# Performance work log

Measured on AMD Instinct MI355X. Metric: run time of the kernel, lower is better.

The kernel has to match this reference:

```python
import jax, jax.numpy as jnp
import numpy as np

B, S, D = 4, 2048, 1024
R = 64
N_FQK = N_FV = N_RQK = N_RV = 32
N_HEADS = 16
D_HEAD = D // N_HEADS


def setup_inputs() -> dict:
    key = jax.random.key(0)
    ks = jax.random.split(key, 10)

    def orth_bank(k, n, rows, cols):
        # mimic per-slice orthogonal init
        a = jax.random.normal(k, (n, rows, cols), dtype=jnp.float32)
        q, _ = jnp.linalg.qr(a) if rows >= cols else (jnp.swapaxes(jnp.linalg.qr(jnp.swapaxes(a, -1, -2))[0], -1, -2), None)
        return q.astype(jnp.float32)

    return {
        "x": jax.random.normal(ks[0], (B, S, D), dtype=jnp.float32),
        "fqk_weights": jax.random.uniform(ks[1], (B, S, N_FQK), dtype=jnp.float32),
        "fv_weights": jax.random.uniform(ks[2], (B, S, N_FV), dtype=jnp.float32),
        "rqk_weights_Q": jax.random.uniform(ks[3], (B, S, N_RQK), dtype=jnp.float32),
        "rqk_weights_K": jax.random.uniform(ks[4], (B, S, N_RQK), dtype=jnp.float32),
        "rv_weights": jax.random.uniform(ks[5], (B, S, N_RV), dtype=jnp.float32),
        "f_neurons": orth_bank(ks[6], N_FQK + N_FV, D, R),   # (64, D, R)
        "r_neurons": orth_bank(ks[7], N_RQK + N_RV, R, D),   # (64, R, D)
        "W_O": jax.random.normal(ks[8], (D, D), dtype=jnp.float32) * (1.0 / np.sqrt(D)),
    }


def reference(x, fqk_weights, fv_weights, rqk_weights_Q, rqk_weights_K, rv_weights,
              f_neurons, r_neurons, W_O):
    fqk = f_neurons[:N_FQK]          # (N, D, R)
    fv = f_neurons[N_FQK:]
    rqk = r_neurons[:N_RQK]          # (N, R, D)
    rv = r_neurons[N_RQK:]

    # Fused routed low-rank projections (same math as bsn,ndr->bsdr then bsd,bsdr->bsr,
    # reassociated to avoid the (B,S,D,R) intermediate).
    h_qk = jnp.einsum('bsd,bsn,ndr->bsr', x, fqk_weights, fqk)
    h_v = jnp.einsum('bsd,bsn,ndr->bsr', x, fv_weights, fv)

    Q = jnp.einsum('bsr,bsn,nrd->bsd', h_qk, rqk_weights_Q, rqk)
    K = jnp.einsum('bsr,bsn,nrd->bsd', h_qk, rqk_weights_K, rqk)
    V = jnp.einsum('bsr,bsn,nrd->bsd', h_v, rv_weights, rv)

    def heads(t):  # (B,S,D) -> (B,H,S,Dh)
        return t.reshape(B, S, N_HEADS, D_HEAD).transpose(0, 2, 1, 3)

    Qh, Kh, Vh = heads(Q), heads(K), heads(V)
    scores = jnp.einsum('bhqd,bhkd->bhqk', Qh, Kh) / np.sqrt(D_HEAD).astype(np.float32)
    causal = jnp.triu(jnp.ones((S, S), dtype=bool), k=1)
    scores = jnp.where(causal[None, None], -jnp.inf, scores)
    attn = jax.nn.softmax(scores, axis=-1)
    attn_out = jnp.einsum('bhqk,bhkd->bhqd', attn, Vh)
    attn_out = attn_out.transpose(0, 2, 1, 3).reshape(B, S, D)
    return attn_out @ W_O.T
```

## Files before the change

kernel.cpp:

```cpp
#include <hip/hip_runtime.h>
#include <hip/hip_bf16.h>


namespace {
constexpr int kS = 2048;
constexpr int kD = 1024;
}

typedef unsigned short u16;
typedef __attribute__((ext_vector_type(2))) float f32x2;
typedef __attribute__((ext_vector_type(4))) float f32x4;
typedef __attribute__((ext_vector_type(8))) short s8v;

union FragU { s8v s; unsigned u[4]; };
union F4U { f32x4 v; f32x2 p[2]; };

__device__ __forceinline__ u16 f2bf_bits(float f) {
  union { float f; unsigned u; } cv; cv.f = f;
  unsigned u = cv.u;
  unsigned r = u + 0x7fffu + ((u >> 16) & 1u);
  return (u16)(r >> 16);
}
__device__ __forceinline__ float bf2f(u16 b) {
  union { unsigned u; float f; } cv; cv.u = ((unsigned)b) << 16; return cv.f;
}
__device__ __forceinline__ unsigned pk_bf16(float a, float b) {
  __hip_bfloat162 h = __float22bfloat162_rn(make_float2(a, b));
  union { __hip_bfloat162 h; unsigned u; } cv; cv.h = h; return cv.u;
}
__device__ __forceinline__ void gl_lds16(const void* g, void* l) {
  __builtin_amdgcn_global_load_lds(
      (const __attribute__((address_space(1))) unsigned int*)g,
      (__attribute__((address_space(3))) unsigned int*)l, 16, 0, 0);
}

__global__ __launch_bounds__(256) void prep(
    const float* __restrict__ x, u16* __restrict__ xb,
    const float* __restrict__ f, u16* __restrict__ FT,
    const float* __restrict__ rn, u16* __restrict__ RT) {
  __shared__ float Tt[128 * 68];
  const int tid = threadIdx.x;
  const int bx = blockIdx.x;

  if (bx < 512) {
    float* T1 = Tt;
    const int d0 = (bx & 7) * 128;
    const int n  = bx >> 3;
#pragma unroll
    for (int e = 0; e < 8; ++e) {
      int flat = tid + e * 256;
      int dd = flat >> 4, r4 = (flat & 15) * 4;
      float4 v = *(const float4*)&f[((size_t)n * kD + d0 + dd) * 64 + r4];
      T1[(r4 + 0) * 132 + dd] = v.x;
      T1[(r4 + 1) * 132 + dd] = v.y;
      T1[(r4 + 2) * 132 + dd] = v.z;
      T1[(r4 + 3) * 132 + dd] = v.w;
    }
    __syncthreads();
#pragma unroll
    for (int e = 0; e < 4; ++e) {
      int flat = tid + e * 256;
      int r = flat >> 4, dq = (flat & 15) * 8;
      const float* p = &T1[r * 132 + dq];
      uint4 o = { pk_bf16(p[0], p[1]), pk_bf16(p[2], p[3]),
                  pk_bf16(p[4], p[5]), pk_bf16(p[6], p[7]) };
      *(uint4*)&FT[((size_t)n * 64 + r) * kD + d0 + dq] = o;
    }
  } else if (bx < 1024) {
    const int b2 = bx - 512;
    const int d0 = (b2 & 7) * 128;
    const int n  = b2 >> 3;
#pragma unroll
    for (int e = 0; e < 8; ++e) {
      int flat = tid + e * 256;
      int r = flat >> 5, d4 = (flat & 31) * 4;
      float4 v = *(const float4*)&rn[((size_t)n * 64 + r) * kD + d0 + d4];
      Tt[(d4 + 0) * 68 + r] = v.x;
      Tt[(d4 + 1) * 68 + r] = v.y;
      Tt[(d4 + 2) * 68 + r] = v.z;
      Tt[(d4 + 3) * 68 + r] = v.w;
    }
    __syncthreads();
#pragma unroll
    for (int e = 0; e < 4; ++e) {
      int flat = tid + e * 256;
      int dd = flat >> 3, rq = (flat & 7) * 8;
      const float* p = &Tt[dd * 68 + rq];
      uint4 o = { pk_bf16(p[0], p[1]), pk_bf16(p[2], p[3]),
                  pk_bf16(p[4], p[5]), pk_bf16(p[6], p[7]) };
      *(uint4*)&RT[((size_t)(d0 + dd)) * 4096 + n * 64 + rq] = o;
    }
  } else {
    int idx = (bx - 1024) * 256 + tid;
    float4 v0 = ((const float4*)x)[idx * 2];
    float4 v1 = ((const float4*)x)[idx * 2 + 1];
    uint4 o = { pk_bf16(v0.x, v0.y), pk_bf16(v0.z, v0.w),
                pk_bf16(v1.x, v1.y), pk_bf16(v1.z, v1.w) };
    ((uint4*)xb)[idx] = o;
  }
}

__global__ __launch_bounds__(256) void g_gemm(const u16* __restrict__ xb,
                                              const u16* __restrict__ FT,
                                              u16* __restrict__ G) {
  __shared__ short As[128 * 64];
  __shared__ short Bs[128 * 64];
  const int tid = threadIdx.x;
  const int lane = tid & 63, wid = tid >> 6;
  const int wm = wid & 1, wn = wid >> 1;
  const int quad = lane >> 4, l15 = lane & 15;
  const int cT = blockIdx.x * 128;
  const int tok0 = blockIdx.y * 128;

  f32x4 acc[4][4];
#pragma unroll
  for (int mt = 0; mt < 4; ++mt)
#pragma unroll
    for (int nt = 0; nt < 4; ++nt) acc[mt][nt] = {0.f, 0.f, 0.f, 0.f};

#pragma unroll 1
  for (int d0 = 0; d0 < kD; d0 += 64) {
    __syncthreads();
#pragma unroll
    for (int e = 0; e < 4; ++e) {
      int flat = tid + e * 256;
      int r = flat >> 3, u = (flat & 7) ^ (r & 7);
      gl_lds16(&xb[(size_t)(tok0 + r) * kD + d0 + u * 8], &As[flat * 8]);
    }
#pragma unroll
    for (int e = 0; e < 4; ++e) {
      int flat = tid + e * 256;
      int r = flat >> 3, u = (flat & 7) ^ (r & 7);
      gl_lds16(&FT[(size_t)(cT + r) * kD + d0 + u * 8], &Bs[flat * 8]);
    }
    __syncthreads();
    s8v a0[4], a1[4], b0[4], b1[4];
#pragma unroll
    for (int mt = 0; mt < 4; ++mt) {
      int r = wm * 64 + mt * 16 + l15;
      a0[mt] = *(const s8v*)&As[r * 64 + ((quad) ^ (r & 7)) * 8];
      a1[mt] = *(const s8v*)&As[r * 64 + ((4 + quad) ^ (r & 7)) * 8];
    }
#pragma unroll
    for (int nt = 0; nt < 4; ++nt) {
      int r = wn * 64 + nt * 16 + l15;
      b0[nt] = *(const s8v*)&Bs[r * 64 + ((quad) ^ (r & 7)) * 8];
      b1[nt] = *(const s8v*)&Bs[r * 64 + ((4 + quad) ^ (r & 7)) * 8];
    }
#pragma unroll
    for (int mt = 0; mt < 4; ++mt)
#pragma unroll
      for (int nt = 0; nt < 4; ++nt) {
        acc[mt][nt] = __builtin_amdgcn_mfma_f32_16x16x32_bf16(
            a0[mt], b0[nt], acc[mt][nt], 0, 0, 0);
        acc[mt][nt] = __builtin_amdgcn_mfma_f32_16x16x32_bf16(
            a1[mt], b1[nt], acc[mt][nt], 0, 0, 0);
      }
  }
#pragma unroll
  for (int mt = 0; mt < 4; ++mt)
#pragma unroll
    for (int nt = 0; nt < 4; ++nt) {
      int col = cT + wn * 64 + nt * 16 + l15;
      int rbase = tok0 + wm * 64 + mt * 16 + quad * 4;
#pragma unroll
      for (int i = 0; i < 4; ++i)
        G[(size_t)(rbase + i) * 4096 + col] = f2bf_bits(acc[mt][nt][i]);
    }
}

__global__ __launch_bounds__(256) void reduce_h_wo(
    const u16* __restrict__ G, const float* __restrict__ fqk_w,
    const float* __restrict__ fv_w, float* __restrict__ h_qk,
    float* __restrict__ h_v, const float* __restrict__ WO,
    u16* __restrict__ wob) {
  const int bx = blockIdx.x;
  if (bx < 512) {
    int idx = bx * 256 + threadIdx.x;
    int t = idx >> 4, r4 = (idx & 15) * 4;
    float4 aq = {0.f, 0.f, 0.f, 0.f}, av = {0.f, 0.f, 0.f, 0.f};
    const u16* gq = &G[(size_t)t * 4096 + r4];
    const u16* gv = gq + 2048;
#pragma unroll 4
    for (int n = 0; n < 32; ++n) {
      float wa = fqk_w[t * 32 + n];
      float wb = fv_w[t * 32 + n];
      ushort4 g1 = *(const ushort4*)&gq[n * 64];
      ushort4 g2 = *(const ushort4*)&gv[n * 64];
      aq.x += wa * bf2f(g1.x); aq.y += wa * bf2f(g1.y);
      aq.z += wa * bf2f(g1.z); aq.w += wa * bf2f(g1.w);
      av.x += wb * bf2f(g2.x); av.y += wb * bf2f(g2.y);
      av.z += wb * bf2f(g2.z); av.w += wb * bf2f(g2.w);
    }
    *(float4*)&h_qk[t * 64 + r4] = aq;
    *(float4*)&h_v[t * 64 + r4] = av;
  } else {
    int idx = (bx - 512) * 256 + threadIdx.x;
    float4 v0 = ((const float4*)WO)[idx * 2];
    float4 v1 = ((const float4*)WO)[idx * 2 + 1];
    uint4 o = { pk_bf16(v0.x, v0.y), pk_bf16(v0.z, v0.w),
                pk_bf16(v1.x, v1.y), pk_bf16(v1.z, v1.w) };
    ((uint4*)wob)[idx] = o;
  }
}

__global__ __launch_bounds__(256) void qkv_gemm(
    const float* __restrict__ h_qk, const float* __restrict__ h_v,
    const float* __restrict__ wq, const float* __restrict__ wk,
    const float* __restrict__ wv, const u16* __restrict__ RT,
    u16* __restrict__ Qb, u16* __restrict__ Kb, u16* __restrict__ VTg) {
  __shared__ float hs[128 * 68];
  __shared__ float wsl[128 * 33];
  short* Bs = (short*)hs;
  const int tid = threadIdx.x;
  const int lane = tid & 63, wid = tid >> 6;
  const int quad = lane >> 4, l15 = lane & 15;
  const int dT = blockIdx.x * 128;
  const int tok0 = blockIdx.y * 128;
  const int which = blockIdx.z;
  const float* __restrict__ h = (which == 2) ? h_v : h_qk;
  const float* __restrict__ w = (which == 0) ? wq : (which == 1) ? wk : wv;
  const int g0 = (which == 2) ? 2048 : 0;

#pragma unroll
  for (int e = 0; e < 8; ++e) {
    int flat = tid + e * 256;
    int row = flat >> 4, rq = (flat & 15) * 4;
    *(float4*)&hs[row * 68 + rq] =
        *(const float4*)&h[(size_t)(tok0 + row) * 64 + rq];
  }
#pragma unroll
  for (int e = 0; e < 16; ++e) {
    int flat = tid + e * 256;
    int row = flat >> 5, nn = flat & 31;
    wsl[row * 33 + nn] = w[(size_t)(tok0 + row) * 32 + nn];
  }
  __syncthreads();

  f32x4 hreg[2][4];
#pragma unroll
  for (int mt = 0; mt < 2; ++mt) {
    const float* hp = &hs[(wid * 32 + mt * 16 + l15) * 68 + quad * 8];
    hreg[mt][0] = *(const f32x4*)hp;
    hreg[mt][1] = *(const f32x4*)(hp + 4);
    hreg[mt][2] = *(const f32x4*)(hp + 32);
    hreg[mt][3] = *(const f32x4*)(hp + 36);
  }

  f32x4 acc[2][8];
#pragma unroll
  for (int mt = 0; mt < 2; ++mt)
#pragma unroll
    for (int nt = 0; nt < 8; ++nt) acc[mt][nt] = {0.f, 0.f, 0.f, 0.f};

#pragma unroll 1
  for (int n = 0; n < 32; ++n) {
    __syncthreads();
#pragma unroll
    for (int e = 0; e < 4; ++e) {
      int flat = tid + e * 256;
      int r = flat >> 3, u = (flat & 7) ^ (r & 7);
      gl_lds16(&RT[(size_t)(dT + r) * 4096 + g0 + n * 64 + u * 8],
               &Bs[flat * 8]);
    }
    __syncthreads();
    s8v a0[2], a1[2], b0[8], b1[8];
#pragma unroll
    for (int mt = 0; mt < 2; ++mt) {
      float wv_ = wsl[(wid * 32 + mt * 16 + l15) * 33 + n];
      f32x2 w2 = {wv_, wv_};
      F4U h0, h1, h2, h3;
      h0.v = hreg[mt][0]; h1.v = hreg[mt][1];
      h2.v = hreg[mt][2]; h3.v = hreg[mt][3];
      f32x2 a00 = w2 * h0.p[0], a01 = w2 * h0.p[1];
      f32x2 a10 = w2 * h1.p[0], a11 = w2 * h1.p[1];
      f32x2 a20 = w2 * h2.p[0], a21 = w2 * h2.p[1];
      f32x2 a30 = w2 * h3.p[0], a31 = w2 * h3.p[1];
      FragU fa, fb;
      fa.u[0] = pk_bf16(a00[0], a00[1]);
      fa.u[1] = pk_bf16(a01[0], a01[1]);
      fa.u[2] = pk_bf16(a10[0], a10[1]);
      fa.u[3] = pk_bf16(a11[0], a11[1]);
      a0[mt] = fa.s;
      fb.u[0] = pk_bf16(a20[0], a20[1]);
      fb.u[1] = pk_bf16(a21[0], a21[1]);
      fb.u[2] = pk_bf16(a30[0], a30[1]);
      fb.u[3] = pk_bf16(a31[0], a31[1]);
      a1[mt] = fb.s;
    }
#pragma unroll
    for (int nt = 0; nt < 8; ++nt) {
      int r = nt * 16 + l15;
      b0[nt] = *(const s8v*)&Bs[r * 64 + ((quad) ^ (r & 7)) * 8];
      b1[nt] = *(const s8v*)&Bs[r * 64 + ((4 + quad) ^ (r & 7)) * 8];
    }
#pragma unroll
    for (int mt = 0; mt < 2; ++mt)
#pragma unroll
      for (int nt = 0; nt < 8; ++nt) {
        acc[mt][nt] = __builtin_amdgcn_mfma_f32_16x16x32_bf16(
            a0[mt], b0[nt], acc[mt][nt], 0, 0, 0);
        acc[mt][nt] = __builtin_amdgcn_mfma_f32_16x16x32_bf16(
            a1[mt], b1[nt], acc[mt][nt], 0, 0, 0);
      }
  }

  if (which < 2) {
    u16* __restrict__ O = (which == 0) ? Qb : Kb;
#pragma unroll
    for (int mt = 0; mt < 2; ++mt)
#pragma unroll
      for (int nt = 0; nt < 8; ++nt) {
        int col = dT + nt * 16 + l15;
        int rbase = tok0 + wid * 32 + mt * 16 + quad * 4;
#pragma unroll
        for (int i = 0; i < 4; ++i)
          O[(size_t)(rbase + i) * kD + col] = f2bf_bits(acc[mt][nt][i]);
      }
  } else {
#pragma unroll
    for (int mt = 0; mt < 2; ++mt)
#pragma unroll
      for (int nt = 0; nt < 8; ++nt) {
        int d = dT + nt * 16 + l15;
        int hh = d >> 6, dl = d & 63;
        int t = tok0 + wid * 32 + mt * 16 + quad * 4;
        int bb = t >> 11, sl = t & 2047;
        ushort4 u = { f2bf_bits(acc[mt][nt][0]), f2bf_bits(acc[mt][nt][1]),
                      f2bf_bits(acc[mt][nt][2]), f2bf_bits(acc[mt][nt][3]) };
        *(ushort4*)&VTg[(((size_t)bb * 16 + hh) * 64 + dl) * kS + sl] = u;
      }
  }
}

__global__ __launch_bounds__(512) void attn_mfma(
    const u16* __restrict__ Qb, const u16* __restrict__ Kb,
    const u16* __restrict__ VTg, u16* __restrict__ AOb)
{
  __shared__ short Ks[64 * 72];
  __shared__ short VTs[64 * 72];
  __shared__ short Ps[8][16 * 72];
  const int tid = threadIdx.x;
  const int lane = tid & 63, w = tid >> 6;
  const int quad = lane >> 4, l15 = lane & 15;
  const int qb = (blockIdx.x + blockIdx.y + 4 * blockIdx.z) & 15;
  const int hh = blockIdx.y, b = blockIdx.z;
  const int dh = hh * 64;
  const size_t qrow0 = (size_t)b * kS + (size_t)qb * 128;
  const int ktmax = qb * 2 + 1;
  const u16* __restrict__ vbase = VTg + ((size_t)(b * 16 + hh) * 64) * kS;

  const int prow = tid >> 3;
  const int pd8  = (tid & 7) * 8;

  *(uint4*)&Ks[prow * 72 + pd8] =
      *(const uint4*)&Kb[((size_t)b * kS + prow) * kD + dh + pd8];
  *(uint4*)&VTs[prow * 72 + pd8] =
      *(const uint4*)&vbase[(size_t)prow * kS + pd8];

  const size_t qrow = qrow0 + w * 16 + l15;
  s8v bq0 = *(const s8v*)&Qb[qrow * kD + dh + quad * 8];
  s8v bq1 = *(const s8v*)&Qb[qrow * kD + dh + 32 + quad * 8];
  __syncthreads();

  const int q_g = qb * 128 + w * 16 + l15;
  const int qmax_w = qb * 128 + w * 16 + 15;
  float m = -INFINITY, l = 0.f;
  f32x4 O[4];
#pragma unroll
  for (int dt = 0; dt < 4; ++dt) O[dt] = {0.f, 0.f, 0.f, 0.f};

#pragma unroll 1
  for (int kt = 0; kt <= ktmax; ++kt) {
    uint4 pk, pv;
    if (kt < ktmax) {
      const size_t krn = (size_t)b * kS + (size_t)(kt + 1) * 64;
      pk = *(const uint4*)&Kb[(krn + prow) * kD + dh + pd8];
      pv = *(const uint4*)&vbase[(size_t)prow * kS + (kt + 1) * 64 + pd8];
    }

    if (kt * 64 <= qmax_w) {
      f32x4 st[4];
      __builtin_amdgcn_s_setprio(1);
#pragma unroll
      for (int nt = 0; nt < 4; ++nt) {
        const short* p = &Ks[(nt * 16 + l15) * 72 + quad * 8];
        s8v ak0 = *(const s8v*)p;
        s8v ak1 = *(const s8v*)(p + 32);
        f32x4 z = {0.f, 0.f, 0.f, 0.f};
        z = __builtin_amdgcn_mfma_f32_16x16x32_bf16(ak0, bq0, z, 0, 0, 0);
        st[nt] = __builtin_amdgcn_mfma_f32_16x16x32_bf16(ak1, bq1, z, 0, 0, 0);
      }
      __builtin_amdgcn_s_setprio(0);

      if (kt * 64 + 63 > qb * 128 + w * 16) {
#pragma unroll
        for (int nt = 0; nt < 4; ++nt)
#pragma unroll
          for (int i = 0; i < 4; ++i)
            if (kt * 64 + nt * 16 + quad * 4 + i > q_g) st[nt][i] = -1e30f;
      }

      float pm = -INFINITY;
#pragma unroll
      for (int nt = 0; nt < 4; ++nt)
#pragma unroll
        for (int i = 0; i < 4; ++i) pm = fmaxf(pm, st[nt][i]);
      pm = fmaxf(pm, __shfl_xor(pm, 16, 64));
      pm = fmaxf(pm, __shfl_xor(pm, 32, 64));
      float mn = fmaxf(m, pm);
      float alpha = __expf((m - mn) * 0.125f);
      m = mn;
      float p[4][4];
      float r = 0.f;
#pragma unroll
      for (int nt = 0; nt < 4; ++nt)
#pragma unroll
        for (int i = 0; i < 4; ++i) {
          p[nt][i] = __expf((st[nt][i] - mn) * 0.125f);
          r += p[nt][i];
        }
      r += __shfl_xor(r, 16, 64);
      r += __shfl_xor(r, 32, 64);
      l = l * alpha + r;
#pragma unroll
      for (int dt = 0; dt < 4; ++dt)
#pragma unroll
        for (int i = 0; i < 4; ++i) O[dt][i] *= alpha;

#pragma unroll
      for (int nt = 0; nt < 4; ++nt) {
        uint2 o = { pk_bf16(p[nt][0], p[nt][1]), pk_bf16(p[nt][2], p[nt][3]) };
        *(uint2*)&Ps[w][l15 * 72 + nt * 16 + quad * 4] = o;
      }
      s8v bp0 = *(const s8v*)&Ps[w][l15 * 72 + quad * 8];
      s8v bp1 = *(const s8v*)&Ps[w][l15 * 72 + 32 + quad * 8];
      __builtin_amdgcn_s_setprio(1);
#pragma unroll
      for (int dt = 0; dt < 4; ++dt) {
        const short* p2 = &VTs[(dt * 16 + l15) * 72 + quad * 8];
        s8v av0 = *(const s8v*)p2;
        s8v av1 = *(const s8v*)(p2 + 32);
        O[dt] = __builtin_amdgcn_mfma_f32_16x16x32_bf16(av0, bp0, O[dt], 0, 0, 0);
        O[dt] = __builtin_amdgcn_mfma_f32_16x16x32_bf16(av1, bp1, O[dt], 0, 0, 0);
      }
      __builtin_amdgcn_s_setprio(0);
    }

    __syncthreads();
    if (kt < ktmax) {
      *(uint4*)&Ks[prow * 72 + pd8] = pk;
      *(uint4*)&VTs[prow * 72 + pd8] = pv;
    }
    __syncthreads();
  }

  const float inv = 1.f / l;
  const size_t row = qrow0 + w * 16 + l15;
#pragma unroll
  for (int dt = 0; dt < 4; ++dt) {
    uint2 o = { pk_bf16(O[dt][0] * inv, O[dt][1] * inv),
                pk_bf16(O[dt][2] * inv, O[dt][3] * inv) };
    *(uint2*)&AOb[row * kD + dh + dt * 16 + quad * 4] = o;
  }
}

__global__ __launch_bounds__(256) void wo_gemm(const u16* __restrict__ AOb,
                                               const u16* __restrict__ wob,
                                               float* __restrict__ out) {
  __shared__ short As[128 * 64];
  __shared__ short Bs[128 * 64];
  const int tid = threadIdx.x;
  const int lane = tid & 63, wid = tid >> 6;
  const int wm = wid & 1, wn = wid >> 1;
  const int quad = lane >> 4, l15 = lane & 15;
  const int dT = blockIdx.x * 128;
  const int tok0 = blockIdx.y * 128;

  f32x4 acc[4][4];
#pragma unroll
  for (int mt = 0; mt < 4; ++mt)
#pragma unroll
    for (int nt = 0; nt < 4; ++nt) acc[mt][nt] = {0.f, 0.f, 0.f, 0.f};

#pragma unroll 1
  for (int e0 = 0; e0 < kD; e0 += 64) {
    __syncthreads();
#pragma unroll
    for (int e = 0; e < 4; ++e) {
      int flat = tid + e * 256;
      int r = flat >> 3, u = (flat & 7) ^ (r & 7);
      gl_lds16(&AOb[(size_t)(tok0 + r) * kD + e0 + u * 8], &As[flat * 8]);
    }
#pragma unroll
    for (int e = 0; e < 4; ++e) {
      int flat = tid + e * 256;
      int r = flat >> 3, u = (flat & 7) ^ (r & 7);
      gl_lds16(&wob[(size_t)(dT + r) * kD + e0 + u * 8], &Bs[flat * 8]);
    }
    __syncthreads();
    s8v a0[4], a1[4], b0[4], b1[4];
#pragma unroll
    for (int mt = 0; mt < 4; ++mt) {
      int r = wm * 64 + mt * 16 + l15;
      a0[mt] = *(const s8v*)&As[r * 64 + ((quad) ^ (r & 7)) * 8];
      a1[mt] = *(const s8v*)&As[r * 64 + ((4 + quad) ^ (r & 7)) * 8];
    }
#pragma unroll
    for (int nt = 0; nt < 4; ++nt) {
      int r = wn * 64 + nt * 16 + l15;
      b0[nt] = *(const s8v*)&Bs[r * 64 + ((quad) ^ (r & 7)) * 8];
      b1[nt] = *(const s8v*)&Bs[r * 64 + ((4 + quad) ^ (r & 7)) * 8];
    }
#pragma unroll
    for (int mt = 0; mt < 4; ++mt)
#pragma unroll
      for (int nt = 0; nt < 4; ++nt) {
        acc[mt][nt] = __builtin_amdgcn_mfma_f32_16x16x32_bf16(
            a0[mt], b0[nt], acc[mt][nt], 0, 0, 0);
        acc[mt][nt] = __builtin_amdgcn_mfma_f32_16x16x32_bf16(
            a1[mt], b1[nt], acc[mt][nt], 0, 0, 0);
      }
  }
#pragma unroll
  for (int mt = 0; mt < 4; ++mt)
#pragma unroll
    for (int nt = 0; nt < 4; ++nt) {
      int col = dT + wn * 64 + nt * 16 + l15;
      int rbase = tok0 + wm * 64 + mt * 16 + quad * 4;
#pragma unroll
      for (int i = 0; i < 4; ++i)
        out[(size_t)(rbase + i) * kD + col] = acc[mt][nt][i];
    }
}

extern "C" void kernel_launch(void* const* d_in, const int* in_sizes, int n_in,
                              void* d_out, int out_size, void* d_ws, size_t ws_size,
                              hipStream_t stream) {
  const float* x     = (const float*)d_in[0];
  const float* fqk_w = (const float*)d_in[1];
  const float* fv_w  = (const float*)d_in[2];
  const float* wq    = (const float*)d_in[3];
  const float* wk    = (const float*)d_in[4];
  const float* wv    = (const float*)d_in[5];
  const float* f_neu = (const float*)d_in[6];
  const float* r_neu = (const float*)d_in[7];
  const float* WO    = (const float*)d_in[8];
  float* out = (float*)d_out;

  char* ws = (char*)d_ws;
  u16*   FT   = (u16*)  (ws);
  u16*   RT   = (u16*)  (ws + ((size_t)8u  << 20));
  u16*   G    = (u16*)  (ws + ((size_t)16u << 20));
  float* h_qk = (float*)(ws + ((size_t)80u << 20));
  float* h_v  = (float*)(ws + ((size_t)82u << 20));
  u16*   Qb   = (u16*)  (ws + ((size_t)16u << 20));
  u16*   Kb   = (u16*)  (ws + ((size_t)32u << 20));
  u16*   VTg  = (u16*)  (ws + ((size_t)48u << 20));
  u16*   AOb  = (u16*)  (ws + ((size_t)64u << 20));
  u16*   xb   = (u16*)  (ws + ((size_t)84u << 20));
  u16*   wob  = (u16*)  (ws + ((size_t)84u << 20));

  hipLaunchKernelGGL(prep, dim3(5120), dim3(256), 0, stream,
                     x, xb, f_neu, FT, r_neu, RT);
  hipLaunchKernelGGL(g_gemm, dim3(32, 64), dim3(256), 0, stream, xb, FT, G);
  hipLaunchKernelGGL(reduce_h_wo, dim3(1024), dim3(256), 0, stream,
                     G, fqk_w, fv_w, h_qk, h_v, WO, wob);
  hipLaunchKernelGGL(qkv_gemm, dim3(8, 64, 3), dim3(256), 0, stream,
                     h_qk, h_v, wq, wk, wv, RT, Qb, Kb, VTg);
  hipLaunchKernelGGL(attn_mfma, dim3(16, 16, 4), dim3(512), 0, stream,
                     Qb, Kb, VTg, AOb);
  hipLaunchKernelGGL(wo_gemm, dim3(8, 64), dim3(256), 0, stream,
                     AOb, wob, out);
}
```

Measured before the change: 446.4 us.

## Fuse routed-weight reduction into g_gemm epilogue with float atomics

The g_gemm epilogue now multiplies each accumulator by its per-token routing weight and atomically adds it into h_qk/h_v. This replaces writing the full bf16 G intermediate and re-reading it in a separate reduce kernel. The h buffers are zeroed by extra blocks in prep, and the W_O bf16 conversion moves into a fourth z-slice of qkv_gemm, which saves one launch. In exchange it issues many contended global float atomics, about 32 adds per output element, and the summation order becomes nondeterministic.

```diff
diff --git a/kernel.cpp b/kernel.cpp
--- a/kernel.cpp
+++ b/kernel.cpp
@@ -37,7 +37,8 @@
 __global__ __launch_bounds__(256) void prep(
     const float* __restrict__ x, u16* __restrict__ xb,
     const float* __restrict__ f, u16* __restrict__ FT,
-    const float* __restrict__ rn, u16* __restrict__ RT) {
+    const float* __restrict__ rn, u16* __restrict__ RT,
+    float* __restrict__ hz) {
   __shared__ float Tt[128 * 68];
   const int tid = threadIdx.x;
   const int bx = blockIdx.x;
@@ -90,19 +91,23 @@
                   pk_bf16(p[4], p[5]), pk_bf16(p[6], p[7]) };
       *(uint4*)&RT[((size_t)(d0 + dd)) * 4096 + n * 64 + rq] = o;
     }
-  } else {
+  } else if (bx < 5120) {
     int idx = (bx - 1024) * 256 + tid;
     float4 v0 = ((const float4*)x)[idx * 2];
     float4 v1 = ((const float4*)x)[idx * 2 + 1];
     uint4 o = { pk_bf16(v0.x, v0.y), pk_bf16(v0.z, v0.w),
                 pk_bf16(v1.x, v1.y), pk_bf16(v1.z, v1.w) };
     ((uint4*)xb)[idx] = o;
-  }
-}
-
-__global__ __launch_bounds__(256) void g_gemm(const u16* __restrict__ xb,
-                                              const u16* __restrict__ FT,
-                                              u16* __restrict__ G) {
+  } else {
+    int idx = (bx - 5120) * 256 + tid;
+    ((float4*)hz)[idx] = make_float4(0.f, 0.f, 0.f, 0.f);
+  }
+}
+
+__global__ __launch_bounds__(256) void g_gemm(
+    const u16* __restrict__ xb, const u16* __restrict__ FT,
+    const float* __restrict__ fqk_w, const float* __restrict__ fv_w,
+    float* __restrict__ h_qk, float* __restrict__ h_v) {
   __shared__ short As[128 * 64];
   __shared__ short Bs[128 * 64];
   const int tid = threadIdx.x;
@@ -157,67 +162,50 @@
             a1[mt], b1[nt], acc[mt][nt], 0, 0, 0);
       }
   }
+
+  const int gcol = cT + wn * 64;
+  const bool isv = gcol >= 2048;
+  const int nn = (isv ? gcol - 2048 : gcol) >> 6;
+  const float* __restrict__ W = isv ? fv_w : fqk_w;
+  float* __restrict__ H = isv ? h_v : h_qk;
 #pragma unroll
   for (int mt = 0; mt < 4; ++mt)
 #pragma unroll
-    for (int nt = 0; nt < 4; ++nt) {
-      int col = cT + wn * 64 + nt * 16 + l15;
-      int rbase = tok0 + wm * 64 + mt * 16 + quad * 4;
-#pragma unroll
-      for (int i = 0; i < 4; ++i)
-        G[(size_t)(rbase + i) * 4096 + col] = f2bf_bits(acc[mt][nt][i]);
-    }
-}
-
-__global__ __launch_bounds__(256) void reduce_h_wo(
-    const u16* __restrict__ G, const float* __restrict__ fqk_w,
-    const float* __restrict__ fv_w, float* __restrict__ h_qk,
-    float* __restrict__ h_v, const float* __restrict__ WO,
-    u16* __restrict__ wob) {
-  const int bx = blockIdx.x;
-  if (bx < 512) {
-    int idx = bx * 256 + threadIdx.x;
-    int t = idx >> 4, r4 = (idx & 15) * 4;
-    float4 aq = {0.f, 0.f, 0.f, 0.f}, av = {0.f, 0.f, 0.f, 0.f};
-    const u16* gq = &G[(size_t)t * 4096 + r4];
-    const u16* gv = gq + 2048;
-#pragma unroll 4
-    for (int n = 0; n < 32; ++n) {
-      float wa = fqk_w[t * 32 + n];
-      float wb = fv_w[t * 32 + n];
-      ushort4 g1 = *(const ushort4*)&gq[n * 64];
-      ushort4 g2 = *(const ushort4*)&gv[n * 64];
-      aq.x += wa * bf2f(g1.x); aq.y += wa * bf2f(g1.y);
-      aq.z += wa * bf2f(g1.z); aq.w += wa * bf2f(g1.w);
-      av.x += wb * bf2f(g2.x); av.y += wb * bf2f(g2.y);
-      av.z += wb * bf2f(g2.z); av.w += wb * bf2f(g2.w);
-    }
-    *(float4*)&h_qk[t * 64 + r4] = aq;
-    *(float4*)&h_v[t * 64 + r4] = av;
-  } else {
-    int idx = (bx - 512) * 256 + threadIdx.x;
+    for (int i = 0; i < 4; ++i) {
+      int t = tok0 + wm * 64 + mt * 16 + quad * 4 + i;
+      float wv = W[t * 32 + nn];
+#pragma unroll
+      for (int nt = 0; nt < 4; ++nt)
+        atomicAdd(&H[(size_t)t * 64 + nt * 16 + l15], wv * acc[mt][nt][i]);
+    }
+}
+
+__global__ __launch_bounds__(256) void qkv_gemm(
+    const float* __restrict__ h_qk, const float* __restrict__ h_v,
+    const float* __restrict__ wq, const float* __restrict__ wk,
+    const float* __restrict__ wv, const u16* __restrict__ RT,
+    u16* __restrict__ Qb, u16* __restrict__ Kb, u16* __restrict__ VTg,
+    const float* __restrict__ WO, u16* __restrict__ wob) {
+  __shared__ float hs[128 * 68];
+  __shared__ float wsl[128 * 33];
+  short* Bs = (short*)hs;
+  const int tid = threadIdx.x;
+  const int which = blockIdx.z;
+
+  if (which == 3) {
+    int idx = (blockIdx.y * 8 + blockIdx.x) * 256 + tid;
     float4 v0 = ((const float4*)WO)[idx * 2];
     float4 v1 = ((const float4*)WO)[idx * 2 + 1];
     uint4 o = { pk_bf16(v0.x, v0.y), pk_bf16(v0.z, v0.w),
                 pk_bf16(v1.x, v1.y), pk_bf16(v1.z, v1.w) };
     ((uint4*)wob)[idx] = o;
-  }
-}
-
-__global__ __launch_bounds__(256) void qkv_gemm(
-    const float* __restrict__ h_qk, const float* __restrict__ h_v,
-    const float* __restrict__ wq, const float* __restrict__ wk,
-    const float* __restrict__ wv, const u16* __restrict__ RT,
-    u16* __restrict__ Qb, u16* __restrict__ Kb, u16* __restrict__ VTg) {
-  __shared__ float hs[128 * 68];
-  __shared__ float wsl[128 * 33];
-  short* Bs = (short*)hs;
-  const int tid = threadIdx.x;
+    return;
+  }
+
   const int lane = tid & 63, wid = tid >> 6;
   const int quad = lane >> 4, l15 = lane & 15;
   const int dT = blockIdx.x * 128;
   const int tok0 = blockIdx.y * 128;
-  const int which = blockIdx.z;
   const float* __restrict__ h = (which == 2) ? h_v : h_qk;
   const float* __restrict__ w = (which == 0) ? wq : (which == 1) ? wk : wv;
   const int g0 = (which == 2) ? 2048 : 0;
@@ -551,7 +539,6 @@
   char* ws = (char*)d_ws;
   u16*   FT   = (u16*)  (ws);
   u16*   RT   = (u16*)  (ws + ((size_t)8u  << 20));
-  u16*   G    = (u16*)  (ws + ((size_t)16u << 20));
   float* h_qk = (float*)(ws + ((size_t)80u << 20));
   float* h_v  = (float*)(ws + ((size_t)82u << 20));
   u16*   Qb   = (u16*)  (ws + ((size_t)16u << 20));
@@ -561,13 +548,12 @@
   u16*   xb   = (u16*)  (ws + ((size_t)84u << 20));
   u16*   wob  = (u16*)  (ws + ((size_t)84u << 20));
 
-  hipLaunchKernelGGL(prep, dim3(5120), dim3(256), 0, stream,
-                     x, xb, f_neu, FT, r_neu, RT);
-  hipLaunchKernelGGL(g_gemm, dim3(32, 64), dim3(256), 0, stream, xb, FT, G);
-  hipLaunchKernelGGL(reduce_h_wo, dim3(1024), dim3(256), 0, stream,
-                     G, fqk_w, fv_w, h_qk, h_v, WO, wob);
-  hipLaunchKernelGGL(qkv_gemm, dim3(8, 64, 3), dim3(256), 0, stream,
-                     h_qk, h_v, wq, wk, wv, RT, Qb, Kb, VTg);
+  hipLaunchKernelGGL(prep, dim3(6144), dim3(256), 0, stream,
+                     x, xb, f_neu, FT, r_neu, RT, h_qk);
+  hipLaunchKernelGGL(g_gemm, dim3(32, 64), dim3(256), 0, stream,
+                     xb, FT, fqk_w, fv_w, h_qk, h_v);
+  hipLaunchKernelGGL(qkv_gemm, dim3(8, 64, 4), dim3(256), 0, stream,
+                     h_qk, h_v, wq, wk, wv, RT, Qb, Kb, VTg, WO, wob);
   hipLaunchKernelGGL(attn_mfma, dim3(16, 16, 4), dim3(512), 0, stream,
                      Qb, Kb, VTg, AOb);
   hipLaunchKernelGGL(wo_gemm, dim3(8, 64), dim3(256), 0, stream,
```

After: 549.9 us. +23.2%, slower.
